# Kernel optimization log

Hardware: AMD Instinct MI355X
Metric: run time of the kernel (lower is better)

## Reference

```python
import jax, jax.numpy as jnp
import numpy as np
import math

NUM_FRAMES = 8
NUM_JOINTS = 22
SEQ = NUM_FRAMES * NUM_JOINTS  # 176
D_MODEL = 256
HEADS = 8
HEAD_DIM = 32
NEG = -9e15


def _pos_embedding(ft_size):
    # att_type == 'spatial': position index = joint id repeated per frame
    pos = jnp.tile(jnp.arange(NUM_JOINTS, dtype=jnp.float32), NUM_FRAMES)[:, None]  # [176,1]
    div = jnp.exp(jnp.arange(0, ft_size, 2, dtype=jnp.float32) * (-math.log(10000.0) / ft_size))
    pe = jnp.zeros((SEQ, ft_size), dtype=jnp.float32)
    pe = pe.at[:, 0::2].set(jnp.sin(pos * div))
    pe = pe.at[:, 1::2].set(jnp.cos(pos * div))
    return pe  # [176, ft_size]


def _spatial_mask():
    # block-diagonal ones, block size NUM_JOINTS
    return jnp.kron(jnp.eye(NUM_FRAMES, dtype=jnp.float32),
                    jnp.ones((NUM_JOINTS, NUM_JOINTS), dtype=jnp.float32))  # [176,176]


def setup_inputs() -> dict:
    key = jax.random.key(0)
    ks = jax.random.split(key, 4)
    scale = 1.0 / math.sqrt(D_MODEL)
    x = jax.random.normal(ks[0], (512, SEQ, D_MODEL), dtype=jnp.float32)
    wq = jax.random.normal(ks[1], (D_MODEL, D_MODEL), dtype=jnp.float32) * scale
    wk = jax.random.normal(ks[2], (D_MODEL, D_MODEL), dtype=jnp.float32) * scale
    wv = jax.random.normal(ks[3], (D_MODEL, D_MODEL), dtype=jnp.float32) * scale
    bq = jnp.zeros((D_MODEL,), dtype=jnp.float32)
    bk = jnp.zeros((D_MODEL,), dtype=jnp.float32)
    bv = jnp.zeros((D_MODEL,), dtype=jnp.float32)
    return {"x": x, "wq": wq, "bq": bq, "wk": wk, "bk": bk, "wv": wv, "bv": bv}


def reference(x, wq, bq, wk, bk, wv, bv):
    bs, s, d = x.shape
    # positional encoding (spatial)
    x = x + _pos_embedding(d)[None, :, :]
    # QKV projections (torch Linear: y = x @ W.T + b), dropout is identity (p=0)
    def proj(w, b):
        y = jnp.einsum('bsd,ed->bse', x, w) + b
        return y.reshape(bs, s, HEADS, HEAD_DIM).transpose(0, 2, 1, 3)  # [B,H,S,Dh]
    q, k, v = proj(wq, bq), proj(wk, bk), proj(wv, bv)
    scores = jnp.einsum('bhqd,bhkd->bhqk', q, k) / math.sqrt(HEAD_DIM)
    m = _spatial_mask()  # [S,S], binary
    scores = scores * m + (1.0 - m) * NEG
    attn = jax.nn.softmax(scores, axis=-1)
    out = jnp.einsum('bhqk,bhkd->bhqd', attn, v)
    return out.transpose(0, 2, 1, 3).reshape(bs, s, HEADS * HEAD_DIM)
```

## Files before the change

kernel.cpp:

```cpp
#include <hip/hip_runtime.h>

#define TOKENS 90112
#define DM 256
#define NOUT 768
#define JOINTS 22

typedef __attribute__((ext_vector_type(8))) short bf16x8;
typedef __attribute__((ext_vector_type(4))) float f32x4;

__device__ __forceinline__ float b2f(unsigned short u) {
    union { unsigned int i; float f; } x; x.i = ((unsigned int)u) << 16; return x.f;
}
__device__ __forceinline__ unsigned short f2b(float f) {
    union { float f; unsigned int u; } x; x.f = f;
    unsigned int r = x.u + 0x7FFFu + ((x.u >> 16) & 1u);
    return (unsigned short)(r >> 16);
}

#define OFF_PEWB 0
#define OFF_WCAN (JOINTS * NOUT * 4)
#define OFF_QKV  (OFF_WCAN + 3 * DM * DM * 2)

__global__ __launch_bounds__(256) void wconv_kernel(const float* __restrict__ w0,
                                                    const float* __restrict__ w1,
                                                    const float* __restrict__ w2,
                                                    unsigned short* __restrict__ wcan)
{
    const float* w = (blockIdx.y == 0) ? w0 : (blockIdx.y == 1 ? w1 : w2);
    int i = (blockIdx.x * 256 + threadIdx.x) * 8;
    const float* s = w + i;
    union { uint4 v; float f[4]; } a, b;
    a.v = *(const uint4*)(s);
    b.v = *(const uint4*)(s + 4);
    union { uint4 v; unsigned short u[8]; } o;
    #pragma unroll
    for (int k = 0; k < 4; ++k) { o.u[k] = f2b(a.f[k]); o.u[4 + k] = f2b(b.f[k]); }
    *(uint4*)(wcan + blockIdx.y * (DM * DM) + i) = o.v;
}

__global__ __launch_bounds__(256) void pewb_kernel(const float* __restrict__ wq,
                                                   const float* __restrict__ wk,
                                                   const float* __restrict__ wv,
                                                   const float* __restrict__ bq,
                                                   const float* __restrict__ bk,
                                                   const float* __restrict__ bv,
                                                   float* __restrict__ pewb)
{
    __shared__ float pe_s[DM];
    const int j   = blockIdx.x / 3;
    const int mat = blockIdx.x % 3;
    const int t = threadIdx.x;
    {
        int i = t >> 1;
        float div = __expf((float)(2 * i) * (-9.210340371976184f / 256.0f));
        float ang = (float)j * div;
        pe_s[t] = (t & 1) ? cosf(ang) : sinf(ang);
    }
    __syncthreads();
    const float* w  = (mat == 0) ? wq : (mat == 1 ? wk : wv);
    const float* bb = (mat == 0) ? bq : (mat == 1 ? bk : bv);
    float acc = bb[t];
    const float* wr = w + (size_t)t * DM;
    #pragma unroll 8
    for (int d = 0; d < DM; ++d) acc += pe_s[d] * wr[d];
    pewb[j * NOUT + mat * DM + t] = acc;
}

#define BM 64
#define BN 128

__global__ __launch_bounds__(256) void qkv_gemm(const float* __restrict__ x,
                                                const unsigned short* __restrict__ wcan,
                                                const float* __restrict__ pewb,
                                                unsigned short* __restrict__ qkv)
{
    __shared__ __align__(16) unsigned short As[BM * 256];
    __shared__ __align__(16) unsigned short Bs[BN * 64];

    const int t    = threadIdx.x;
    const int m0   = blockIdx.x * BM;
    const int lane = t & 63;
    const int wave = t >> 6;
    const int wm   = (wave & 1) * 32;
    const int wn   = (wave >> 1) * 64;
    const int lrow = lane & 15;
    const int quad = lane >> 4;

    #pragma unroll
    for (int i = 0; i < 8; ++i) {
        int ch  = t + i * 256;
        int row = ch >> 5, c = ch & 31;
        const float* src = x + (size_t)(m0 + row) * DM + c * 8;
        union { uint4 v; float f[4]; } a, b;
        a.v = *(const uint4*)(src);
        b.v = *(const uint4*)(src + 4);
        union { uint4 v; unsigned short u[8]; } o;
        #pragma unroll
        for (int k = 0; k < 4; ++k) { o.u[k] = f2b(a.f[k]); o.u[4 + k] = f2b(b.f[k]); }
        int cs = (c & 24) | ((c & 7) ^ (row & 7));
        *(uint4*)(&As[row * 256 + cs * 8]) = o.v;
    }

    for (int bn = 0; bn < 6; ++bn) {
        const unsigned short* wbase = wcan + (bn >> 1) * (DM * DM) + (bn & 1) * (BN * DM);

        f32x4 acc[2][4];
        #pragma unroll
        for (int mi = 0; mi < 2; ++mi)
            #pragma unroll
            for (int ni = 0; ni < 4; ++ni)
                acc[mi][ni] = (f32x4){0.f, 0.f, 0.f, 0.f};

        for (int k0 = 0; k0 < DM; k0 += 64) {
            __syncthreads();
            #pragma unroll
            for (int i = 0; i < 4; ++i) {
                int ch  = t + i * 256;
                int row = ch >> 3, c = ch & 7;
                uint4 v = *(const uint4*)(&wbase[(size_t)row * DM + k0 + c * 8]);
                *(uint4*)(&Bs[row * 64 + ((c ^ (row & 7)) * 8)]) = v;
            }
            __syncthreads();
            #pragma unroll
            for (int kk = 0; kk < 64; kk += 32) {
                bf16x8 a[2], b[4];
                #pragma unroll
                for (int mi = 0; mi < 2; ++mi) {
                    int row = wm + mi * 16 + lrow;
                    int c   = ((k0 + kk) >> 3) + quad;
                    int cs  = (c & 24) | ((c & 7) ^ (row & 7));
                    a[mi] = *(const bf16x8*)(&As[row * 256 + cs * 8]);
                }
                #pragma unroll
                for (int ni = 0; ni < 4; ++ni) {
                    int row = wn + ni * 16 + lrow;
                    int c   = (kk >> 3) + quad;
                    b[ni] = *(const bf16x8*)(&Bs[row * 64 + ((c ^ (row & 7)) * 8)]);
                }
                #pragma unroll
                for (int mi = 0; mi < 2; ++mi)
                    #pragma unroll
                    for (int ni = 0; ni < 4; ++ni)
                        acc[mi][ni] = __builtin_amdgcn_mfma_f32_16x16x32_bf16(
                            a[mi], b[ni], acc[mi][ni], 0, 0, 0);
            }
        }

        const int n0 = bn * BN;
        #pragma unroll
        for (int mi = 0; mi < 2; ++mi) {
            #pragma unroll
            for (int r = 0; r < 4; ++r) {
                int row   = wm + mi * 16 + quad * 4 + r;
                int token = m0 + row;
                int joint = token % JOINTS;
                const float* pw = pewb + joint * NOUT + n0;
                size_t obase = (size_t)token * NOUT + n0;
                #pragma unroll
                for (int ni = 0; ni < 4; ++ni) {
                    int col = wn + ni * 16 + lrow;
                    qkv[obase + col] = f2b(acc[mi][ni][r] + pw[col]);
                }
            }
        }
    }
}

#define KVSTR 712
#define OSTR 260

__global__ __launch_bounds__(256) void attn_kernel(const unsigned short* __restrict__ qkv,
                                                   float* __restrict__ out)
{
    __shared__ __align__(16) char smem_raw[JOINTS * OSTR * 4];
    unsigned short* kv  = (unsigned short*)smem_raw;
    float*          o_s = (float*)smem_raw;

    const int t  = threadIdx.x;
    const int tb = blockIdx.x * JOINTS;

    for (int i = t; i < JOINTS * 64; i += 256) {
        int j  = i >> 6;
        int cc = i & 63;
        int e  = 256 + cc * 8;
        int mat = e >> 8;
        int h  = (e >> 5) & 7;
        int d0 = e & 31;
        uint4 v = *(const uint4*)(&qkv[(size_t)(tb + j) * NOUT + e]);
        *(uint4*)(&kv[(mat - 1) * (8 * KVSTR) + h * KVSTR + j * 32 + d0]) = v;
    }
    __syncthreads();

    const bool active = (t < 176);
    float o[32];
    if (active) {
        const int h  = t / 22;
        const int qi = t - h * 22;
        const int token = tb + qi;

        float q[32];
        {
            const unsigned short* qg = qkv + (size_t)token * NOUT + h * 32;
            #pragma unroll
            for (int c4 = 0; c4 < 4; ++c4) {
                union { uint4 v; unsigned short u[8]; } r;
                r.v = *(const uint4*)(qg + c4 * 8);
                #pragma unroll
                for (int ii = 0; ii < 8; ++ii)
                    q[c4 * 8 + ii] = b2f(r.u[ii]) * 0.17677669529663688f;
            }
        }
        const unsigned short* kh = kv + h * KVSTR;
        const unsigned short* vh = kv + 8 * KVSTR + h * KVSTR;

        float sc[22];
        float mx = -3.0e38f;
        #pragma unroll
        for (int j = 0; j < 22; ++j) {
            const unsigned short* kr = kh + j * 32;
            float s = 0.f;
            #pragma unroll
            for (int d = 0; d < 32; ++d) s += q[d] * b2f(kr[d]);
            sc[j] = s;
            mx = fmaxf(mx, s);
        }
        float sum = 0.f;
        #pragma unroll
        for (int j = 0; j < 22; ++j) { sc[j] = __expf(sc[j] - mx); sum += sc[j]; }
        float inv = 1.f / sum;

        #pragma unroll
        for (int d = 0; d < 32; ++d) o[d] = 0.f;
        #pragma unroll
        for (int j = 0; j < 22; ++j) {
            float p = sc[j] * inv;
            const unsigned short* vr = vh + j * 32;
            #pragma unroll
            for (int d = 0; d < 32; ++d) o[d] += p * b2f(vr[d]);
        }
    }
    __syncthreads();

    if (active) {
        const int h  = t / 22;
        const int qi = t - h * 22;
        float* od = o_s + qi * OSTR + h * 32;
        #pragma unroll
        for (int k = 0; k < 8; ++k)
            *(float4*)(od + k * 4) = make_float4(o[k * 4], o[k * 4 + 1], o[k * 4 + 2], o[k * 4 + 3]);
    }
    __syncthreads();

    float* gbase = out + (size_t)tb * DM;
    for (int i4 = t; i4 < JOINTS * 64; i4 += 256) {
        int row = i4 >> 6;
        int col = (i4 & 63) * 4;
        *(float4*)(gbase + i4 * 4) = *(const float4*)(o_s + row * OSTR + col);
    }
}

extern "C" void kernel_launch(void* const* d_in, const int* in_sizes, int n_in,
                              void* d_out, int out_size, void* d_ws, size_t ws_size,
                              hipStream_t stream) {
    const float* x  = (const float*)d_in[0];
    const float* wq = (const float*)d_in[1];
    const float* bq = (const float*)d_in[2];
    const float* wk = (const float*)d_in[3];
    const float* bk = (const float*)d_in[4];
    const float* wv = (const float*)d_in[5];
    const float* bv = (const float*)d_in[6];

    char* ws = (char*)d_ws;
    float*          pewb = (float*)(ws + OFF_PEWB);
    unsigned short* wcan = (unsigned short*)(ws + OFF_WCAN);
    unsigned short* qkv  = (unsigned short*)(ws + OFF_QKV);

    wconv_kernel<<<dim3(32, 3), dim3(256), 0, stream>>>(wq, wk, wv, wcan);
    pewb_kernel<<<dim3(66), dim3(256), 0, stream>>>(wq, wk, wv, bq, bk, bv, pewb);
    qkv_gemm<<<dim3(TOKENS / BM), dim3(256), 0, stream>>>(x, wcan, pewb, qkv);
    attn_kernel<<<dim3(TOKENS / JOINTS), dim3(256), 0, stream>>>(qkv, (float*)d_out);
}
```

Before: 319.4 us.

## Fuse QKV projection and per-frame attention into one kernel

Replaces the separate QKV GEMM and attention kernels with one fused kernel. Each block handles 88 tokens (four frames) and loops over head pairs, computing Q/K/V for two heads with MFMA into shared memory, then running attention from LDS. Two threads share each query row and combine partial dot products with a shuffle. This removes the bf16 QKV round trip through global memory and a kernel launch. In exchange, weights are read directly from global/L2 without LDS staging, and wave tiles are padded (clamped rows), which wastes some MFMA work.

```diff
diff --git a/kernel.cpp b/kernel.cpp
--- a/kernel.cpp
+++ b/kernel.cpp
@@ -1,15 +1,23 @@
 #include <hip/hip_runtime.h>
 
-#define TOKENS 90112
 #define DM 256
 #define NOUT 768
 #define JOINTS 22
+#define MROWS 88
+#define QSTR 40
+#define NBLK 1024
 
 typedef __attribute__((ext_vector_type(8))) short bf16x8;
 typedef __attribute__((ext_vector_type(4))) float f32x4;
 
 __device__ __forceinline__ float b2f(unsigned short u) {
     union { unsigned int i; float f; } x; x.i = ((unsigned int)u) << 16; return x.f;
+}
+__device__ __forceinline__ float blo(unsigned int w) {
+    union { unsigned int i; float f; } x; x.i = w << 16; return x.f;
+}
+__device__ __forceinline__ float bhi(unsigned int w) {
+    union { unsigned int i; float f; } x; x.i = w & 0xFFFF0000u; return x.f;
 }
 __device__ __forceinline__ unsigned short f2b(float f) {
     union { float f; unsigned int u; } x; x.f = f;
@@ -19,7 +27,6 @@
 
 #define OFF_PEWB 0
 #define OFF_WCAN (JOINTS * NOUT * 4)
-#define OFF_QKV  (OFF_WCAN + 3 * DM * DM * 2)
 
 __global__ __launch_bounds__(256) void wconv_kernel(const float* __restrict__ w0,
                                                     const float* __restrict__ w1,
@@ -66,31 +73,22 @@
     pewb[j * NOUT + mat * DM + t] = acc;
 }
 
-#define BM 64
-#define BN 128
-
-__global__ __launch_bounds__(256) void qkv_gemm(const float* __restrict__ x,
-                                                const unsigned short* __restrict__ wcan,
-                                                const float* __restrict__ pewb,
-                                                unsigned short* __restrict__ qkv)
+__global__ __launch_bounds__(512, 4) void fused_kernel(const float* __restrict__ x,
+                                                       const unsigned short* __restrict__ wcan,
+                                                       const float* __restrict__ pewb,
+                                                       float* __restrict__ out)
 {
-    __shared__ __align__(16) unsigned short As[BM * 256];
-    __shared__ __align__(16) unsigned short Bs[BN * 64];
+    __shared__ __align__(16) unsigned short xs[MROWS * 256];
+    __shared__ __align__(16) unsigned short q_s[2 * MROWS * QSTR];
+    __shared__ __align__(16) unsigned short k_s[2 * MROWS * 32];
+    __shared__ __align__(16) unsigned short v_s[2 * MROWS * 32];
 
     const int t    = threadIdx.x;
-    const int m0   = blockIdx.x * BM;
-    const int lane = t & 63;
-    const int wave = t >> 6;
-    const int wm   = (wave & 1) * 32;
-    const int wn   = (wave >> 1) * 64;
-    const int lrow = lane & 15;
-    const int quad = lane >> 4;
-
-    #pragma unroll
-    for (int i = 0; i < 8; ++i) {
-        int ch  = t + i * 256;
-        int row = ch >> 5, c = ch & 31;
-        const float* src = x + (size_t)(m0 + row) * DM + c * 8;
+    const int tok0 = blockIdx.x * MROWS;
+
+    for (int i = t; i < MROWS * 32; i += 512) {
+        int row = i >> 5, c = i & 31;
+        const float* src = x + (size_t)(tok0 + row) * DM + c * 8;
         union { uint4 v; float f[4]; } a, b;
         a.v = *(const uint4*)(src);
         b.v = *(const uint4*)(src + 4);
@@ -98,164 +96,167 @@
         #pragma unroll
         for (int k = 0; k < 4; ++k) { o.u[k] = f2b(a.f[k]); o.u[4 + k] = f2b(b.f[k]); }
         int cs = (c & 24) | ((c & 7) ^ (row & 7));
-        *(uint4*)(&As[row * 256 + cs * 8]) = o.v;
-    }
-
-    for (int bn = 0; bn < 6; ++bn) {
-        const unsigned short* wbase = wcan + (bn >> 1) * (DM * DM) + (bn & 1) * (BN * DM);
-
-        f32x4 acc[2][4];
-        #pragma unroll
-        for (int mi = 0; mi < 2; ++mi)
-            #pragma unroll
-            for (int ni = 0; ni < 4; ++ni)
+        *(uint4*)(&xs[row * 256 + cs * 8]) = o.v;
+    }
+    __syncthreads();
+
+    const int lane = t & 63;
+    const int wave = t >> 6;
+    const int wm   = (wave & 1) * 48;
+    const int wn   = (wave >> 1) * 48;
+    const int lrow = lane & 15;
+    const int quad = lane >> 4;
+
+    int abase[3], axor[3];
+    #pragma unroll
+    for (int mi = 0; mi < 3; ++mi) {
+        int ar = wm + mi * 16 + lrow;
+        if (ar > MROWS - 1) ar = MROWS - 1;
+        abase[mi] = ar * 256;
+        axor[mi]  = ar & 7;
+    }
+
+    for (int it = 0; it < 4; ++it) {
+        const int h0 = it * 2;
+
+        const unsigned short* bp[3];
+        #pragma unroll
+        for (int ni = 0; ni < 3; ++ni) {
+            int n   = wn + ni * 16 + lrow;
+            int mat = n >> 6;
+            int e   = (h0 + ((n >> 5) & 1)) * 32 + (n & 31);
+            bp[ni] = wcan + mat * (DM * DM) + (size_t)e * DM + quad * 8;
+        }
+
+        f32x4 acc[3][3];
+        #pragma unroll
+        for (int mi = 0; mi < 3; ++mi)
+            #pragma unroll
+            for (int ni = 0; ni < 3; ++ni)
                 acc[mi][ni] = (f32x4){0.f, 0.f, 0.f, 0.f};
 
-        for (int k0 = 0; k0 < DM; k0 += 64) {
-            __syncthreads();
-            #pragma unroll
-            for (int i = 0; i < 4; ++i) {
-                int ch  = t + i * 256;
-                int row = ch >> 3, c = ch & 7;
-                uint4 v = *(const uint4*)(&wbase[(size_t)row * DM + k0 + c * 8]);
-                *(uint4*)(&Bs[row * 64 + ((c ^ (row & 7)) * 8)]) = v;
-            }
-            __syncthreads();
-            #pragma unroll
-            for (int kk = 0; kk < 64; kk += 32) {
-                bf16x8 a[2], b[4];
-                #pragma unroll
-                for (int mi = 0; mi < 2; ++mi) {
-                    int row = wm + mi * 16 + lrow;
-                    int c   = ((k0 + kk) >> 3) + quad;
-                    int cs  = (c & 24) | ((c & 7) ^ (row & 7));
-                    a[mi] = *(const bf16x8*)(&As[row * 256 + cs * 8]);
-                }
-                #pragma unroll
-                for (int ni = 0; ni < 4; ++ni) {
-                    int row = wn + ni * 16 + lrow;
-                    int c   = (kk >> 3) + quad;
-                    b[ni] = *(const bf16x8*)(&Bs[row * 64 + ((c ^ (row & 7)) * 8)]);
-                }
-                #pragma unroll
-                for (int mi = 0; mi < 2; ++mi)
+        #pragma unroll
+        for (int kk = 0; kk < DM; kk += 32) {
+            bf16x8 a[3], b[3];
+            #pragma unroll
+            for (int mi = 0; mi < 3; ++mi) {
+                int c  = (kk >> 3) + quad;
+                int cs = (c & 24) | ((c & 7) ^ axor[mi]);
+                a[mi] = *(const bf16x8*)(&xs[abase[mi] + cs * 8]);
+            }
+            #pragma unroll
+            for (int ni = 0; ni < 3; ++ni)
+                b[ni] = *(const bf16x8*)(bp[ni] + kk);
+            #pragma unroll
+            for (int mi = 0; mi < 3; ++mi)
+                #pragma unroll
+                for (int ni = 0; ni < 3; ++ni)
+                    acc[mi][ni] = __builtin_amdgcn_mfma_f32_16x16x32_bf16(
+                        a[mi], b[ni], acc[mi][ni], 0, 0, 0);
+        }
+
+        __syncthreads();
+
+        #pragma unroll
+        for (int ni = 0; ni < 3; ++ni) {
+            int n   = wn + ni * 16 + lrow;
+            int mat = n >> 6;
+            int hl  = (n >> 5) & 1;
+            int d   = n & 31;
+            int pcol = mat * 256 + (h0 + hl) * 32 + d;
+            unsigned short* dst;
+            int str;
+            if (mat == 0)      { dst = &q_s[(hl * MROWS) * QSTR + d]; str = QSTR; }
+            else if (mat == 1) { dst = &k_s[(hl * MROWS) * 32 + d];   str = 32; }
+            else               { dst = &v_s[(hl * MROWS) * 32 + d];   str = 32; }
+            #pragma unroll
+            for (int mi = 0; mi < 3; ++mi) {
+                int rbase = wm + mi * 16 + quad * 4;
+                if (rbase < MROWS) {
                     #pragma unroll
-                    for (int ni = 0; ni < 4; ++ni)
-                        acc[mi][ni] = __builtin_amdgcn_mfma_f32_16x16x32_bf16(
-                            a[mi], b[ni], acc[mi][ni], 0, 0, 0);
-            }
-        }
-
-        const int n0 = bn * BN;
-        #pragma unroll
-        for (int mi = 0; mi < 2; ++mi) {
-            #pragma unroll
-            for (int r = 0; r < 4; ++r) {
-                int row   = wm + mi * 16 + quad * 4 + r;
-                int token = m0 + row;
-                int joint = token % JOINTS;
-                const float* pw = pewb + joint * NOUT + n0;
-                size_t obase = (size_t)token * NOUT + n0;
-                #pragma unroll
-                for (int ni = 0; ni < 4; ++ni) {
-                    int col = wn + ni * 16 + lrow;
-                    qkv[obase + col] = f2b(acc[mi][ni][r] + pw[col]);
-                }
-            }
-        }
-    }
-}
-
-#define KVSTR 712
-#define OSTR 260
-
-__global__ __launch_bounds__(256) void attn_kernel(const unsigned short* __restrict__ qkv,
-                                                   float* __restrict__ out)
-{
-    __shared__ __align__(16) char smem_raw[JOINTS * OSTR * 4];
-    unsigned short* kv  = (unsigned short*)smem_raw;
-    float*          o_s = (float*)smem_raw;
-
-    const int t  = threadIdx.x;
-    const int tb = blockIdx.x * JOINTS;
-
-    for (int i = t; i < JOINTS * 64; i += 256) {
-        int j  = i >> 6;
-        int cc = i & 63;
-        int e  = 256 + cc * 8;
-        int mat = e >> 8;
-        int h  = (e >> 5) & 7;
-        int d0 = e & 31;
-        uint4 v = *(const uint4*)(&qkv[(size_t)(tb + j) * NOUT + e]);
-        *(uint4*)(&kv[(mat - 1) * (8 * KVSTR) + h * KVSTR + j * 32 + d0]) = v;
-    }
-    __syncthreads();
-
-    const bool active = (t < 176);
-    float o[32];
-    if (active) {
-        const int h  = t / 22;
-        const int qi = t - h * 22;
-        const int token = tb + qi;
-
-        float q[32];
-        {
-            const unsigned short* qg = qkv + (size_t)token * NOUT + h * 32;
-            #pragma unroll
-            for (int c4 = 0; c4 < 4; ++c4) {
-                union { uint4 v; unsigned short u[8]; } r;
-                r.v = *(const uint4*)(qg + c4 * 8);
-                #pragma unroll
-                for (int ii = 0; ii < 8; ++ii)
-                    q[c4 * 8 + ii] = b2f(r.u[ii]) * 0.17677669529663688f;
-            }
-        }
-        const unsigned short* kh = kv + h * KVSTR;
-        const unsigned short* vh = kv + 8 * KVSTR + h * KVSTR;
-
-        float sc[22];
-        float mx = -3.0e38f;
-        #pragma unroll
-        for (int j = 0; j < 22; ++j) {
-            const unsigned short* kr = kh + j * 32;
-            float s = 0.f;
-            #pragma unroll
-            for (int d = 0; d < 32; ++d) s += q[d] * b2f(kr[d]);
-            sc[j] = s;
-            mx = fmaxf(mx, s);
-        }
-        float sum = 0.f;
-        #pragma unroll
-        for (int j = 0; j < 22; ++j) { sc[j] = __expf(sc[j] - mx); sum += sc[j]; }
-        float inv = 1.f / sum;
-
-        #pragma unroll
-        for (int d = 0; d < 32; ++d) o[d] = 0.f;
-        #pragma unroll
-        for (int j = 0; j < 22; ++j) {
-            float p = sc[j] * inv;
-            const unsigned short* vr = vh + j * 32;
-            #pragma unroll
-            for (int d = 0; d < 32; ++d) o[d] += p * b2f(vr[d]);
-        }
-    }
-    __syncthreads();
-
-    if (active) {
-        const int h  = t / 22;
-        const int qi = t - h * 22;
-        float* od = o_s + qi * OSTR + h * 32;
-        #pragma unroll
-        for (int k = 0; k < 8; ++k)
-            *(float4*)(od + k * 4) = make_float4(o[k * 4], o[k * 4 + 1], o[k * 4 + 2], o[k * 4 + 3]);
-    }
-    __syncthreads();
-
-    float* gbase = out + (size_t)tb * DM;
-    for (int i4 = t; i4 < JOINTS * 64; i4 += 256) {
-        int row = i4 >> 6;
-        int col = (i4 & 63) * 4;
-        *(float4*)(gbase + i4 * 4) = *(const float4*)(o_s + row * OSTR + col);
+                    for (int rg = 0; rg < 4; ++rg) {
+                        int r = rbase + rg;
+                        int joint = r % 22;
+                        float val = acc[mi][ni][rg] + pewb[joint * NOUT + pcol];
+                        dst[r * str] = f2b(val);
+                    }
+                }
+            }
+        }
+        __syncthreads();
+
+        if (t < 2 * 2 * MROWS) {
+            const int rid = t >> 1;
+            const int dh  = (t & 1) << 4;
+            const int hl  = (rid >= MROWS) ? 1 : 0;
+            const int r   = rid - hl * MROWS;
+            const int fr  = r / 22;
+
+            float q[16];
+            {
+                const unsigned short* qp = &q_s[(hl * MROWS + r) * QSTR + dh];
+                union { uint4 v; unsigned int w[4]; } a0, a1;
+                a0.v = *(const uint4*)(qp);
+                a1.v = *(const uint4*)(qp + 8);
+                #pragma unroll
+                for (int i = 0; i < 4; ++i) {
+                    q[2 * i]     = blo(a0.w[i]) * 0.17677669529663688f;
+                    q[2 * i + 1] = bhi(a0.w[i]) * 0.17677669529663688f;
+                    q[8 + 2 * i]     = blo(a1.w[i]) * 0.17677669529663688f;
+                    q[8 + 2 * i + 1] = bhi(a1.w[i]) * 0.17677669529663688f;
+                }
+            }
+
+            const unsigned short* kp = &k_s[(hl * MROWS + fr * 22) * 32 + dh];
+            float sc[22];
+            float mx = -3.0e38f;
+            #pragma unroll
+            for (int j = 0; j < 22; ++j) {
+                union { uint4 v; unsigned int w[4]; } a0, a1;
+                a0.v = *(const uint4*)(kp + j * 32);
+                a1.v = *(const uint4*)(kp + j * 32 + 8);
+                float s = 0.f;
+                #pragma unroll
+                for (int i = 0; i < 4; ++i) {
+                    s += q[2 * i]     * blo(a0.w[i]);
+                    s += q[2 * i + 1] * bhi(a0.w[i]);
+                    s += q[8 + 2 * i]     * blo(a1.w[i]);
+                    s += q[8 + 2 * i + 1] * bhi(a1.w[i]);
+                }
+                s += __shfl_xor(s, 1);
+                sc[j] = s;
+                mx = fmaxf(mx, s);
+            }
+            float sum = 0.f;
+            #pragma unroll
+            for (int j = 0; j < 22; ++j) { sc[j] = __expf(sc[j] - mx); sum += sc[j]; }
+            float inv = 1.f / sum;
+
+            float o[16];
+            #pragma unroll
+            for (int d = 0; d < 16; ++d) o[d] = 0.f;
+            const unsigned short* vp = &v_s[(hl * MROWS + fr * 22) * 32 + dh];
+            #pragma unroll
+            for (int j = 0; j < 22; ++j) {
+                float p = sc[j] * inv;
+                union { uint4 v; unsigned int w[4]; } a0, a1;
+                a0.v = *(const uint4*)(vp + j * 32);
+                a1.v = *(const uint4*)(vp + j * 32 + 8);
+                #pragma unroll
+                for (int i = 0; i < 4; ++i) {
+                    o[2 * i]     += p * blo(a0.w[i]);
+                    o[2 * i + 1] += p * bhi(a0.w[i]);
+                    o[8 + 2 * i]     += p * blo(a1.w[i]);
+                    o[8 + 2 * i + 1] += p * bhi(a1.w[i]);
+                }
+            }
+
+            float* op = out + (size_t)(tok0 + r) * DM + ((h0 + hl) << 5) + dh;
+            *(float4*)(op)      = make_float4(o[0],  o[1],  o[2],  o[3]);
+            *(float4*)(op + 4)  = make_float4(o[4],  o[5],  o[6],  o[7]);
+            *(float4*)(op + 8)  = make_float4(o[8],  o[9],  o[10], o[11]);
+            *(float4*)(op + 12) = make_float4(o[12], o[13], o[14], o[15]);
+        }
     }
 }
 
@@ -273,10 +274,8 @@
     char* ws = (char*)d_ws;
     float*          pewb = (float*)(ws + OFF_PEWB);
     unsigned short* wcan = (unsigned short*)(ws + OFF_WCAN);
-    unsigned short* qkv  = (unsigned short*)(ws + OFF_QKV);
 
     wconv_kernel<<<dim3(32, 3), dim3(256), 0, stream>>>(wq, wk, wv, wcan);
     pewb_kernel<<<dim3(66), dim3(256), 0, stream>>>(wq, wk, wv, bq, bk, bv, pewb);
-    qkv_gemm<<<dim3(TOKENS / BM), dim3(256), 0, stream>>>(x, wcan, pewb, qkv);
-    attn_kernel<<<dim3(TOKENS / JOINTS), dim3(256), 0, stream>>>(qkv, (float*)d_out);
-}
+    fused_kernel<<<dim3(NBLK), dim3(512), 0, stream>>>(x, wcan, pewb, (float*)d_out);
+}
```

Result: slower. 838.5 us (+162.5%).

## Double-buffer weight tiles in QKV GEMM and move attention to MFMA

Applied to the files above, without the earlier changes.

The QKV GEMM now double-buffers the weight tile in shared memory. The next K-slice, or the first slice of the next N block, is prefetched into registers while MFMAs run on the current buffer, which drops one barrier per step. The attention kernel is rewritten to process two frames per block and compute QK^T and PV with bf16 MFMA instructions instead of scalar per-thread loops. V is stored transposed and zero-padded in shared memory, and softmax uses lane shuffles. This adds bf16 rounding of the probabilities and clamped or padded rows, which could cost some accuracy.

```diff
diff --git a/kernel.cpp b/kernel.cpp
--- a/kernel.cpp
+++ b/kernel.cpp
@@ -75,7 +75,7 @@
                                                 unsigned short* __restrict__ qkv)
 {
     __shared__ __align__(16) unsigned short As[BM * 256];
-    __shared__ __align__(16) unsigned short Bs[BN * 64];
+    __shared__ __align__(16) unsigned short Bs[2][BN * 64];
 
     const int t    = threadIdx.x;
     const int m0   = blockIdx.x * BM;
@@ -101,6 +101,16 @@
         *(uint4*)(&As[row * 256 + cs * 8]) = o.v;
     }
 
+    #pragma unroll
+    for (int i = 0; i < 4; ++i) {
+        int ch = t + i * 256;
+        int row = ch >> 3, c = ch & 7;
+        uint4 v = *(const uint4*)(&wcan[(size_t)row * DM + c * 8]);
+        *(uint4*)(&Bs[0][row * 64 + ((c ^ (row & 7)) * 8)]) = v;
+    }
+    __syncthreads();
+
+    #pragma unroll 1
     for (int bn = 0; bn < 6; ++bn) {
         const unsigned short* wbase = wcan + (bn >> 1) * (DM * DM) + (bn & 1) * (BN * DM);
 
@@ -111,31 +121,39 @@
             for (int ni = 0; ni < 4; ++ni)
                 acc[mi][ni] = (f32x4){0.f, 0.f, 0.f, 0.f};
 
-        for (int k0 = 0; k0 < DM; k0 += 64) {
-            __syncthreads();
-            #pragma unroll
-            for (int i = 0; i < 4; ++i) {
-                int ch  = t + i * 256;
-                int row = ch >> 3, c = ch & 7;
-                uint4 v = *(const uint4*)(&wbase[(size_t)row * DM + k0 + c * 8]);
-                *(uint4*)(&Bs[row * 64 + ((c ^ (row & 7)) * 8)]) = v;
-            }
-            __syncthreads();
-            #pragma unroll
-            for (int kk = 0; kk < 64; kk += 32) {
+        #pragma unroll 1
+        for (int k0i = 0; k0i < 4; ++k0i) {
+            const int cur = k0i & 1;
+            const bool pf = (k0i < 3) || (bn < 5);
+            const unsigned short* wpf = (k0i < 3) ? wbase
+                : (wcan + ((bn + 1) >> 1) * (DM * DM) + ((bn + 1) & 1) * (BN * DM));
+            const int kpf = (k0i < 3) ? (k0i + 1) * 64 : 0;
+
+            uint4 pr[4];
+            if (pf) {
+                #pragma unroll
+                for (int i = 0; i < 4; ++i) {
+                    int ch = t + i * 256;
+                    int row = ch >> 3, c = ch & 7;
+                    pr[i] = *(const uint4*)(&wpf[(size_t)row * DM + kpf + c * 8]);
+                }
+            }
+
+            #pragma unroll
+            for (int kk2 = 0; kk2 < 2; ++kk2) {
                 bf16x8 a[2], b[4];
                 #pragma unroll
                 for (int mi = 0; mi < 2; ++mi) {
                     int row = wm + mi * 16 + lrow;
-                    int c   = ((k0 + kk) >> 3) + quad;
+                    int c   = ((k0i * 64 + kk2 * 32) >> 3) + quad;
                     int cs  = (c & 24) | ((c & 7) ^ (row & 7));
                     a[mi] = *(const bf16x8*)(&As[row * 256 + cs * 8]);
                 }
                 #pragma unroll
                 for (int ni = 0; ni < 4; ++ni) {
                     int row = wn + ni * 16 + lrow;
-                    int c   = (kk >> 3) + quad;
-                    b[ni] = *(const bf16x8*)(&Bs[row * 64 + ((c ^ (row & 7)) * 8)]);
+                    int cb  = kk2 * 4 + quad;
+                    b[ni] = *(const bf16x8*)(&Bs[cur][row * 64 + ((cb ^ (row & 7)) * 8)]);
                 }
                 #pragma unroll
                 for (int mi = 0; mi < 2; ++mi)
@@ -144,6 +162,16 @@
                         acc[mi][ni] = __builtin_amdgcn_mfma_f32_16x16x32_bf16(
                             a[mi], b[ni], acc[mi][ni], 0, 0, 0);
             }
+
+            if (pf) {
+                #pragma unroll
+                for (int i = 0; i < 4; ++i) {
+                    int ch = t + i * 256;
+                    int row = ch >> 3, c = ch & 7;
+                    *(uint4*)(&Bs[cur ^ 1][row * 64 + ((c ^ (row & 7)) * 8)]) = pr[i];
+                }
+            }
+            __syncthreads();
         }
 
         const int n0 = bn * BN;
@@ -166,96 +194,142 @@
     }
 }
 
-#define KVSTR 712
-#define OSTR 260
+#define ABLK 44
 
 __global__ __launch_bounds__(256) void attn_kernel(const unsigned short* __restrict__ qkv,
                                                    float* __restrict__ out)
 {
-    __shared__ __align__(16) char smem_raw[JOINTS * OSTR * 4];
-    unsigned short* kv  = (unsigned short*)smem_raw;
-    float*          o_s = (float*)smem_raw;
-
-    const int t  = threadIdx.x;
-    const int tb = blockIdx.x * JOINTS;
-
-    for (int i = t; i < JOINTS * 64; i += 256) {
-        int j  = i >> 6;
-        int cc = i & 63;
-        int e  = 256 + cc * 8;
-        int mat = e >> 8;
-        int h  = (e >> 5) & 7;
-        int d0 = e & 31;
-        uint4 v = *(const uint4*)(&qkv[(size_t)(tb + j) * NOUT + e]);
-        *(uint4*)(&kv[(mat - 1) * (8 * KVSTR) + h * KVSTR + j * 32 + d0]) = v;
+    __shared__ __align__(16) unsigned short k_s[8 * ABLK * 40];
+    __shared__ __align__(16) unsigned short v_t[16 * 32 * 24 + 8];
+
+    const int t    = threadIdx.x;
+    const int tok0 = blockIdx.x * ABLK;
+    const int lane = t & 63;
+    const int wave = t >> 6;
+    const int lrow = lane & 15;
+    const int quad = lane >> 4;
+
+    for (int i = t; i < 16 * 32; i += 256)
+        *(unsigned int*)(&v_t[i * 24 + 22]) = 0u;
+    if (t < 4) ((unsigned int*)(&v_t[16 * 32 * 24]))[t] = 0u;
+
+    for (int i = t; i < ABLK * 32; i += 256) {
+        int r = i >> 5;
+        int c = i & 31;
+        int h = c >> 2, dc = c & 3;
+        uint4 v = *(const uint4*)(&qkv[(size_t)(tok0 + r) * NOUT + 256 + c * 8]);
+        *(uint4*)(&k_s[(h * ABLK + r) * 40 + dc * 8]) = v;
+    }
+    for (int i = t; i < ABLK * 32; i += 256) {
+        int r = i >> 5;
+        int c = i & 31;
+        int h = c >> 2, dc = c & 3;
+        int fr = r / 22, k = r - fr * 22;
+        union { uint4 v; unsigned short u[8]; } w;
+        w.v = *(const uint4*)(&qkv[(size_t)(tok0 + r) * NOUT + 512 + c * 8]);
+        int base = ((h * 2 + fr) * 32 + dc * 8) * 24 + k;
+        #pragma unroll
+        for (int j = 0; j < 8; ++j) v_t[base + j * 24] = w.u[j];
     }
     __syncthreads();
 
-    const bool active = (t < 176);
-    float o[32];
-    if (active) {
-        const int h  = t / 22;
-        const int qi = t - h * 22;
-        const int token = tb + qi;
-
-        float q[32];
-        {
-            const unsigned short* qg = qkv + (size_t)token * NOUT + h * 32;
-            #pragma unroll
-            for (int c4 = 0; c4 < 4; ++c4) {
-                union { uint4 v; unsigned short u[8]; } r;
-                r.v = *(const uint4*)(qg + c4 * 8);
-                #pragma unroll
-                for (int ii = 0; ii < 8; ++ii)
-                    q[c4 * 8 + ii] = b2f(r.u[ii]) * 0.17677669529663688f;
-            }
-        }
-        const unsigned short* kh = kv + h * KVSTR;
-        const unsigned short* vh = kv + 8 * KVSTR + h * KVSTR;
-
-        float sc[22];
-        float mx = -3.0e38f;
-        #pragma unroll
-        for (int j = 0; j < 22; ++j) {
-            const unsigned short* kr = kh + j * 32;
-            float s = 0.f;
-            #pragma unroll
-            for (int d = 0; d < 32; ++d) s += q[d] * b2f(kr[d]);
-            sc[j] = s;
-            mx = fmaxf(mx, s);
-        }
-        float sum = 0.f;
-        #pragma unroll
-        for (int j = 0; j < 22; ++j) { sc[j] = __expf(sc[j] - mx); sum += sc[j]; }
-        float inv = 1.f / sum;
-
-        #pragma unroll
-        for (int d = 0; d < 32; ++d) o[d] = 0.f;
-        #pragma unroll
-        for (int j = 0; j < 22; ++j) {
-            float p = sc[j] * inv;
-            const unsigned short* vr = vh + j * 32;
-            #pragma unroll
-            for (int d = 0; d < 32; ++d) o[d] += p * b2f(vr[d]);
-        }
-    }
-    __syncthreads();
-
-    if (active) {
-        const int h  = t / 22;
-        const int qi = t - h * 22;
-        float* od = o_s + qi * OSTR + h * 32;
-        #pragma unroll
-        for (int k = 0; k < 8; ++k)
-            *(float4*)(od + k * 4) = make_float4(o[k * 4], o[k * 4 + 1], o[k * 4 + 2], o[k * 4 + 3]);
-    }
-    __syncthreads();
-
-    float* gbase = out + (size_t)tb * DM;
-    for (int i4 = t; i4 < JOINTS * 64; i4 += 256) {
-        int row = i4 >> 6;
-        int col = (i4 & 63) * 4;
-        *(float4*)(gbase + i4 * 4) = *(const float4*)(o_s + row * OSTR + col);
+    const float SC = 0.17677669529663688f;
+
+    #pragma unroll 1
+    for (int stp = 0; stp < 4; ++stp) {
+        const int u4 = wave + stp * 4;
+        const int fr = u4 & 1;
+        const int h  = u4 >> 1;
+
+        bf16x8 ka[2], qb[2];
+        #pragma unroll
+        for (int km = 0; km < 2; ++km) {
+            int kr = km * 16 + lrow; if (kr > 21) kr = 21;
+            ka[km] = *(const bf16x8*)(&k_s[(h * ABLK + fr * 22 + kr) * 40 + quad * 8]);
+        }
+        #pragma unroll
+        for (int qn = 0; qn < 2; ++qn) {
+            int qr = qn * 16 + lrow; if (qr > 21) qr = 21;
+            qb[qn] = *(const bf16x8*)(&qkv[(size_t)(tok0 + fr * 22 + qr) * NOUT + h * 32 + quad * 8]);
+        }
+        f32x4 st[2][2];
+        #pragma unroll
+        for (int km = 0; km < 2; ++km)
+            #pragma unroll
+            for (int qn = 0; qn < 2; ++qn)
+                st[km][qn] = __builtin_amdgcn_mfma_f32_16x16x32_bf16(
+                    ka[km], qb[qn], (f32x4){0.f, 0.f, 0.f, 0.f}, 0, 0, 0);
+
+        unsigned int u[2][2][2];
+        #pragma unroll
+        for (int qn = 0; qn < 2; ++qn) {
+            float mx = -3.0e38f;
+            #pragma unroll
+            for (int r2 = 0; r2 < 4; ++r2) mx = fmaxf(mx, st[0][qn][r2] * SC);
+            #pragma unroll
+            for (int r2 = 0; r2 < 4; ++r2)
+                if (16 + quad * 4 + r2 < 22) mx = fmaxf(mx, st[1][qn][r2] * SC);
+            mx = fmaxf(mx, __shfl_xor(mx, 16));
+            mx = fmaxf(mx, __shfl_xor(mx, 32));
+            float p0[4], p1[4];
+            float sum = 0.f;
+            #pragma unroll
+            for (int r2 = 0; r2 < 4; ++r2) { p0[r2] = __expf(st[0][qn][r2] * SC - mx); sum += p0[r2]; }
+            #pragma unroll
+            for (int r2 = 0; r2 < 4; ++r2) {
+                float e = (16 + quad * 4 + r2 < 22) ? __expf(st[1][qn][r2] * SC - mx) : 0.f;
+                p1[r2] = e; sum += e;
+            }
+            sum += __shfl_xor(sum, 16);
+            sum += __shfl_xor(sum, 32);
+            float inv = 1.f / sum;
+            #pragma unroll
+            for (int r2 = 0; r2 < 4; ++r2) { p0[r2] *= inv; p1[r2] *= inv; }
+            u[qn][0][0] = (unsigned int)f2b(p0[0]) | ((unsigned int)f2b(p0[1]) << 16);
+            u[qn][0][1] = (unsigned int)f2b(p0[2]) | ((unsigned int)f2b(p0[3]) << 16);
+            u[qn][1][0] = (unsigned int)f2b(p1[0]) | ((unsigned int)f2b(p1[1]) << 16);
+            u[qn][1][1] = (unsigned int)f2b(p1[2]) | ((unsigned int)f2b(p1[3]) << 16);
+        }
+
+        bf16x8 pa[2];
+        #pragma unroll
+        for (int qm = 0; qm < 2; ++qm) {
+            union { bf16x8 v; unsigned int w[4]; } au;
+            #pragma unroll
+            for (int j = 0; j < 4; ++j) {
+                int src = lrow + 16 * ((quad & 1) * 2 + (j >> 1));
+                unsigned int lo = (unsigned int)__shfl((int)u[qm][0][j & 1], src, 64);
+                unsigned int hi = (unsigned int)__shfl((int)u[qm][1][j & 1], src, 64);
+                au.w[j] = (quad < 2) ? lo : hi;
+            }
+            pa[qm] = au.v;
+        }
+
+        bf16x8 vb[2];
+        #pragma unroll
+        for (int dn = 0; dn < 2; ++dn)
+            vb[dn] = *(const bf16x8*)(&v_t[((h * 2 + fr) * 32 + dn * 16 + lrow) * 24 + quad * 8]);
+
+        f32x4 ot[2][2];
+        #pragma unroll
+        for (int qm = 0; qm < 2; ++qm)
+            #pragma unroll
+            for (int dn = 0; dn < 2; ++dn)
+                ot[qm][dn] = __builtin_amdgcn_mfma_f32_16x16x32_bf16(
+                    pa[qm], vb[dn], (f32x4){0.f, 0.f, 0.f, 0.f}, 0, 0, 0);
+
+        #pragma unroll
+        for (int qm = 0; qm < 2; ++qm) {
+            #pragma unroll
+            for (int r2 = 0; r2 < 4; ++r2) {
+                int q = qm * 16 + quad * 4 + r2;
+                if (q < 22) {
+                    float* op = out + (size_t)(tok0 + fr * 22 + q) * DM + h * 32;
+                    op[lrow]      = ot[qm][0][r2];
+                    op[16 + lrow] = ot[qm][1][r2];
+                }
+            }
+        }
     }
 }
 
@@ -278,5 +352,5 @@
     wconv_kernel<<<dim3(32, 3), dim3(256), 0, stream>>>(wq, wk, wv, wcan);
     pewb_kernel<<<dim3(66), dim3(256), 0, stream>>>(wq, wk, wv, bq, bk, bv, pewb);
     qkv_gemm<<<dim3(TOKENS / BM), dim3(256), 0, stream>>>(x, wcan, pewb, qkv);
-    attn_kernel<<<dim3(TOKENS / JOINTS), dim3(256), 0, stream>>>(qkv, (float*)d_out);
-}
+    attn_kernel<<<dim3(TOKENS / ABLK), dim3(256), 0, stream>>>(qkv, (float*)d_out);
+}
```

After: 342.9 us. 7.3% more time.
